# Performance work log

Hardware: AMD Instinct MI355X
Metric: run time of the kernel (lower is better)

The kernel has to match this reference:

```python
import jax, jax.numpy as jnp
import numpy as np

N_NODES = 50000
N_EDGES = 640000
HIDDEN = 128
EDGE_DIM = 32


def _init_linear(key, fan_in, fan_out):
    kw, kb = jax.random.split(key)
    bound = 1.0 / np.sqrt(fan_in)
    W = jax.random.uniform(kw, (fan_in, fan_out), jnp.float32, -bound, bound)
    b = jax.random.uniform(kb, (fan_out,), jnp.float32, -bound, bound)
    return W, b


def setup_inputs() -> dict:
    key = jax.random.key(0)
    ks = jax.random.split(key, 10)
    node_features = jax.random.normal(ks[0], (N_NODES, HIDDEN), jnp.float32)
    edge_index = jax.random.randint(ks[1], (2, N_EDGES), 0, N_NODES, jnp.int64)
    edge_features = jax.random.normal(ks[2], (N_EDGES, EDGE_DIM), jnp.float32)
    coordination = jax.random.uniform(ks[3], (N_NODES,), jnp.float32)
    msg_in = 2 * HIDDEN + EDGE_DIM + 2
    upd_in = 2 * HIDDEN + 1
    mW1, mb1 = _init_linear(ks[4], msg_in, HIDDEN)
    mW2, mb2 = _init_linear(ks[5], HIDDEN, HIDDEN)
    uW1, ub1 = _init_linear(ks[6], upd_in, HIDDEN)
    uW2, ub2 = _init_linear(ks[7], HIDDEN, HIDDEN)
    ln_gamma = jnp.ones((HIDDEN,), jnp.float32)
    ln_beta = jnp.zeros((HIDDEN,), jnp.float32)
    return {
        "node_features": node_features,
        "edge_index": edge_index,
        "edge_features": edge_features,
        "coordination": coordination,
        "mW1": mW1, "mb1": mb1, "mW2": mW2, "mb2": mb2,
        "uW1": uW1, "ub1": ub1, "uW2": uW2, "ub2": ub2,
        "ln_gamma": ln_gamma, "ln_beta": ln_beta,
    }


def _layernorm(x, gamma, beta, eps=1e-5):
    mu = jnp.mean(x, axis=-1, keepdims=True)
    var = jnp.mean(jnp.square(x - mu), axis=-1, keepdims=True)
    return (x - mu) * jax.lax.rsqrt(var + eps) * gamma + beta


def reference(node_features, edge_index, edge_features, coordination,
              mW1, mb1, mW2, mb2, uW1, ub1, uW2, ub2, ln_gamma, ln_beta):
    n_nodes = node_features.shape[0]
    src, dst = edge_index[0], edge_index[1]
    # edge_input: [E, 2H + edge_dim + 2]
    edge_input = jnp.concatenate([
        node_features[src],
        node_features[dst],
        edge_features,
        coordination[src][:, None],
        coordination[dst][:, None],
    ], axis=-1)
    h = jax.nn.silu(edge_input @ mW1 + mb1)
    messages = h @ mW2 + mb2  # [E, H]
    aggregated = jax.ops.segment_sum(messages, dst, num_segments=n_nodes)  # [N, H]
    update_input = jnp.concatenate([
        node_features, aggregated, coordination[:, None]
    ], axis=-1)  # [N, 2H+1]
    u = jax.nn.silu(update_input @ uW1 + ub1)
    upd = u @ uW2 + ub2
    return _layernorm(node_features + upd, ln_gamma, ln_beta)
```

## Files before the change

### kernel.cpp

```cpp
#include <hip/hip_runtime.h>

#define NN 50000
#define NE 640000
#define HID 128


typedef __attribute__((ext_vector_type(8))) short bf8;
typedef __attribute__((ext_vector_type(4))) float f4;

#define MFMA(a, b, c) __builtin_amdgcn_mfma_f32_16x16x32_bf16(a, b, c, 0, 0, 0)

#define SYNC() do { asm volatile("s_waitcnt lgkmcnt(0)" ::: "memory"); \
                    __builtin_amdgcn_s_barrier(); } while (0)

__device__ __forceinline__ short f2bf(float f) {
    union { float f; unsigned u; } v; v.f = f;
    unsigned r = v.u + 0x7FFFu + ((v.u >> 16) & 1u);
    return (short)(r >> 16);
}
__device__ __forceinline__ float bf2f(short s) {
    union { unsigned u; float f; } v; v.u = ((unsigned)(unsigned short)s) << 16;
    return v.f;
}
__device__ __forceinline__ float silu(float x) {
    return x * __builtin_amdgcn_rcpf(1.f + __expf(-x));
}

__global__ __launch_bounds__(256, 2)
void prep_kernel(const float* __restrict__ nf, const float* __restrict__ coord,
                 const float* __restrict__ mW1, const float* __restrict__ mb1,
                 const float* __restrict__ mW2,
                 const float* __restrict__ uW1, const float* __restrict__ uW2,
                 const int* __restrict__ ei,
                 short* __restrict__ W1e, short* __restrict__ W2p,
                 short* __restrict__ U1p, short* __restrict__ U2p,
                 short* __restrict__ Ppre, int* __restrict__ hist) {
    const int b = blockIdx.x, tid = threadIdx.x;
    if (b < 782) {
        __shared__ short SH[64 * 264];
        __shared__ float scoord[64];
        short* A = SH;
        short* P = SH;
        const int nbase = b * 64;

        {
            const int r = tid >> 2, q = tid & 3;
            const int node = nbase + r;
            short* Ar = A + r * 136 + q * 32;
            if (node < NN) {
                const float* p = nf + (long)node * HID + q * 32;
#pragma unroll
                for (int j = 0; j < 4; ++j) {
                    f4 v0 = *(const f4*)(p + j * 8), v1 = *(const f4*)(p + j * 8 + 4);
                    bf8 w = { f2bf(v0[0]), f2bf(v0[1]), f2bf(v0[2]), f2bf(v0[3]),
                              f2bf(v1[0]), f2bf(v1[1]), f2bf(v1[2]), f2bf(v1[3]) };
                    *(bf8*)(Ar + j * 8) = w;
                }
                if (q == 0) scoord[r] = coord[node];
            } else {
                bf8 z = {};
#pragma unroll
                for (int j = 0; j < 4; ++j) *(bf8*)(Ar + j * 8) = z;
                if (q == 0) scoord[r] = 0.f;
            }
        }
        __syncthreads();

        const int lane = tid & 63, wv = tid >> 6;
        const int g = lane >> 4, i16 = lane & 15, wc = wv * 64;

        f4 acc[4][4] = {};
#pragma unroll
        for (int ks = 0; ks < 4; ++ks) {
            const int kb = ks * 32 + g * 8;
            bf8 bfr[4];
#pragma unroll
            for (int n = 0; n < 4; ++n) {
                const int cc = wc + n * 16 + i16;
                const float* wp = mW1 + ((cc >> 7) ? (128 * 128 + (cc - 128)) : cc);
#pragma unroll
                for (int j = 0; j < 8; ++j)
                    bfr[n][j] = f2bf(wp[(kb + j) * 128]);
            }
#pragma unroll
            for (int m = 0; m < 4; ++m) {
                bf8 a = *(const bf8*)(A + (m * 16 + i16) * 136 + kb);
#pragma unroll
                for (int n = 0; n < 4; ++n) acc[m][n] = MFMA(a, bfr[n], acc[m][n]);
            }
        }
        __syncthreads();

#pragma unroll
        for (int n = 0; n < 4; ++n) {
            const int cc = wc + n * 16 + i16;
            const float wa = mW1[(288 + (cc >> 7)) * 128 + (cc & 127)];
            const float ba = (cc >> 7) ? mb1[cc - 128] : 0.f;
#pragma unroll
            for (int m = 0; m < 4; ++m)
#pragma unroll
                for (int i = 0; i < 4; ++i) {
                    const int row = m * 16 + g * 4 + i;
                    P[row * 264 + cc] = f2bf(acc[m][n][i] + scoord[row] * wa + ba);
                }
        }
        __syncthreads();

        {
            const int r = tid >> 2, q = tid & 3;
            const int node = nbase + r;
            if (node < NN) {
#pragma unroll
                for (int j = 0; j < 8; ++j)
                    *(bf8*)(Ppre + (long)node * 256 + q * 64 + j * 8) =
                        *(const bf8*)(P + r * 264 + q * 64 + j * 8);
            }
        }
    } else if (b < 846) {
        const int stride = 64 * 256;
        const int idx = (b - 782) * 256 + tid;
        for (int t = idx; t < 128 * 32; t += stride) {
            int c = t / 32, k = t % 32;
            W1e[t] = f2bf(mW1[(256 + k) * 128 + c]);
        }
        for (int t = idx; t < 128 * 128; t += stride)
            W2p[t] = f2bf(mW2[(t % 128) * 128 + (t / 128)]);
        for (int t = idx; t < 128 * 288; t += stride) {
            int n = t / 288, k = t % 288;
            U1p[t] = (k < 257) ? f2bf(uW1[k * 128 + n]) : (short)0;
        }
        for (int t = idx; t < 128 * 128; t += stride)
            U2p[t] = f2bf(uW2[(t % 128) * 128 + (t / 128)]);
    } else {
        const int stride = 154 * 256;
        for (int e = (b - 846) * 256 + tid; e < NE; e += stride)
            atomicAdd(&hist[ei[NE + e]], 1);
    }
}

__global__ void scan1_kernel(const int* __restrict__ hist, int* __restrict__ pos,
                             int* __restrict__ csum) {
    __shared__ int s[256];
    const int b = blockIdx.x, t = threadIdx.x;
    const int idx = b * 200 + t;
    int v = (t < 200) ? hist[idx] : 0;
    s[t] = v;
    __syncthreads();
    for (int d = 1; d < 256; d <<= 1) {
        int x = (t >= d) ? s[t - d] : 0;
        __syncthreads();
        s[t] += x;
        __syncthreads();
    }
    if (t < 200) pos[idx] = s[t] - v;
    if (t == 255) csum[b] = s[255];
}

__global__ void scan_add_kernel(int* __restrict__ pos, const int* __restrict__ csum) {
    __shared__ int sw[4];
    const int b = blockIdx.x, t = threadIdx.x;
    int v = (t < b) ? csum[t] : 0;
    v += __shfl_xor(v, 1);  v += __shfl_xor(v, 2);  v += __shfl_xor(v, 4);
    v += __shfl_xor(v, 8);  v += __shfl_xor(v, 16); v += __shfl_xor(v, 32);
    if ((t & 63) == 0) sw[t >> 6] = v;
    __syncthreads();
    const int total = sw[0] + sw[1] + sw[2] + sw[3];
    if (t < 200) pos[b * 200 + t] += total;
}

__global__ void scatter_kernel(const int* __restrict__ ei, const float* __restrict__ ef,
                               int* __restrict__ pos, int* __restrict__ srcs,
                               int* __restrict__ dsts, short* __restrict__ efs) {
    const int tid = threadIdx.x;
    const int lane = tid & 63;
    const int r = tid >> 2, q = tid & 3;
#pragma unroll
    for (int k = 0; k < 4; ++k) {
        const int e = (blockIdx.x * 4 + k) * 64 + r;
        int p = 0;
        if (q == 0) {
            const int d = ei[NE + e];
            p = atomicAdd(&pos[d], 1);
            srcs[p] = ei[e];
            dsts[p] = d;
        }
        p = __shfl(p, lane & 60);
        const float* pe = ef + (long)e * 32 + q * 8;
        f4 v0 = *(const f4*)pe, v1 = *(const f4*)(pe + 4);
        bf8 w = { f2bf(v0[0]), f2bf(v0[1]), f2bf(v0[2]), f2bf(v0[3]),
                  f2bf(v1[0]), f2bf(v1[1]), f2bf(v1[2]), f2bf(v1[3]) };
        *(bf8*)(efs + (long)p * 32 + q * 8) = w;
    }
}

__global__ __launch_bounds__(256, 7)
void edge_kernel(const int* __restrict__ srcs, const int* __restrict__ dsts,
                 const short* __restrict__ efs, const short* __restrict__ Ppre,
                 const short* __restrict__ W1e, const short* __restrict__ W2p,
                 const float* __restrict__ mb2, float* __restrict__ agg) {
    constexpr int LDEF = 36, LDH = 136, LDM = 132;
    __shared__ short Aef[64 * LDEF];
    __shared__ short HM[64 * LDH];
    __shared__ int sdst[64], ssrc[64];
    short* H = HM;
    float* Mh = (float*)HM;

    const int tid = threadIdx.x;
    const int bid = blockIdx.x;
    const int ebase = ((bid & 7) * 1250 + (bid >> 3)) * 64;

    const int lane = tid & 63, wv = tid >> 6;
    const int g = lane >> 4, i16 = lane & 15, wc = wv * 32;
    const int r = tid >> 2, q = tid & 3;

    const int e = ebase + r;
    if (q == 0) { sdst[r] = dsts[e]; ssrc[r] = srcs[e]; }
    bf8 ev = *(const bf8*)(efs + (long)e * 32 + q * 8);
    bf8 b0 = *(const bf8*)(W1e + (wc + i16) * 32 + g * 8);
    bf8 b1 = *(const bf8*)(W1e + (wc + 16 + i16) * 32 + g * 8);
    const float c0 = mb2[wc + i16], c1 = mb2[wc + 16 + i16];
    *(bf8*)(Aef + r * LDEF + q * 8) = ev;
    SYNC();

    {
        f4 acc[4][2] = {};
#pragma unroll
        for (int m = 0; m < 4; ++m) {
            bf8 a = *(const bf8*)(Aef + (m * 16 + i16) * LDEF + g * 8);
            acc[m][0] = MFMA(a, b0, acc[m][0]);
            acc[m][1] = MFMA(a, b1, acc[m][1]);
        }
#pragma unroll
        for (int m = 0; m < 4; ++m)
#pragma unroll
            for (int n = 0; n < 2; ++n)
#pragma unroll
                for (int i = 0; i < 4; ++i)
                    H[(m * 16 + g * 4 + i) * LDH + wc + n * 16 + i16] = f2bf(acc[m][n][i]);
    }
    SYNC();

    {
        const int s_ = ssrc[r], d_ = sdst[r];
        const short* p1 = Ppre + (long)s_ * 256 + q * 32;
        const short* p2 = Ppre + (long)d_ * 256 + 128 + q * 32;
        bf8 a1[4], a2[4];
#pragma unroll
        for (int j = 0; j < 4; ++j) a1[j] = *(const bf8*)(p1 + j * 8);
#pragma unroll
        for (int j = 0; j < 4; ++j) a2[j] = *(const bf8*)(p2 + j * 8);
        short* Hr = H + r * LDH + q * 32;
#pragma unroll
        for (int j = 0; j < 4; ++j) {
            bf8 hv = *(const bf8*)(Hr + j * 8);
            bf8 o;
#pragma unroll
            for (int t = 0; t < 8; ++t) {
                float x = bf2f(hv[t]) + bf2f(a1[j][t]) + bf2f(a2[j][t]);
                o[t] = f2bf(silu(x));
            }
            *(bf8*)(Hr + j * 8) = o;
        }
    }
    SYNC();

    f4 acc2[4][2] = {};
#pragma unroll
    for (int ks = 0; ks < 4; ++ks) {
        const int kb = ks * 32 + g * 8;
        bf8 w0 = *(const bf8*)(W2p + (wc + i16) * 128 + kb);
        bf8 w1 = *(const bf8*)(W2p + (wc + 16 + i16) * 128 + kb);
#pragma unroll
        for (int m = 0; m < 4; ++m) {
            bf8 a = *(const bf8*)(H + (m * 16 + i16) * LDH + kb);
            acc2[m][0] = MFMA(a, w0, acc2[m][0]);
            acc2[m][1] = MFMA(a, w1, acc2[m][1]);
        }
    }
    SYNC();

#pragma unroll
    for (int m = 0; m < 2; ++m)
#pragma unroll
        for (int n = 0; n < 2; ++n)
#pragma unroll
            for (int i = 0; i < 4; ++i)
                Mh[(m * 16 + g * 4 + i) * LDM + wc + n * 16 + i16] =
                    acc2[m][n][i] + (n ? c1 : c0);
    SYNC();
    {
        const int col = tid & 127, half = tid >> 7;
        const int base = half * 16;
        float run = 0.f;
#pragma unroll
        for (int rr = 0; rr < 16; ++rr) {
            const int row = base + rr;
            run += Mh[row * LDM + col];
            const bool last = (rr == 15) || (sdst[row + 1] != sdst[row]);
            if (last) {
                atomicAdd(agg + (long)sdst[row] * HID + col, run);
                run = 0.f;
            }
        }
    }
    SYNC();

#pragma unroll
    for (int m = 2; m < 4; ++m)
#pragma unroll
        for (int n = 0; n < 2; ++n)
#pragma unroll
            for (int i = 0; i < 4; ++i)
                Mh[((m - 2) * 16 + g * 4 + i) * LDM + wc + n * 16 + i16] =
                    acc2[m][n][i] + (n ? c1 : c0);
    SYNC();
    {
        const int col = tid & 127, half = tid >> 7;
        const int base = half * 16;
        float run = 0.f;
#pragma unroll
        for (int rr = 0; rr < 16; ++rr) {
            const int row = 32 + base + rr;
            run += Mh[(row - 32) * LDM + col];
            const bool last = (rr == 15) || (row == 63) || (sdst[row + 1] != sdst[row]);
            if (last) {
                atomicAdd(agg + (long)sdst[row] * HID + col, run);
                run = 0.f;
            }
        }
    }
}

__global__ __launch_bounds__(256, 4)
void node_kernel(const float* __restrict__ nf, const float* __restrict__ agg,
                 const float* __restrict__ coord,
                 const short* __restrict__ U1p, const float* __restrict__ ub1,
                 const short* __restrict__ U2p, const float* __restrict__ ub2,
                 const float* __restrict__ gamma, const float* __restrict__ beta,
                 float* __restrict__ out) {
    constexpr int K1 = 288, LDA = 296, LDH = 136, LDX = 132;
    __shared__ short SH[64 * LDA];
    short* A = SH;
    short* H = SH;
    float* X = (float*)SH;

    const int tid = threadIdx.x;
    const int nbase = blockIdx.x * 64;

    {
        const int r = tid >> 2, q = tid & 3;
        const int node = nbase + r;
        short* Ar = A + r * LDA;
        bf8 z = {};
        if (node < NN) {
            const float* pn = nf + (long)node * HID + q * 32;
            const float* pa = agg + (long)node * HID + q * 32;
#pragma unroll
            for (int j = 0; j < 4; ++j) {
                f4 v0 = *(const f4*)(pn + j * 8), v1 = *(const f4*)(pn + j * 8 + 4);
                bf8 w = { f2bf(v0[0]), f2bf(v0[1]), f2bf(v0[2]), f2bf(v0[3]),
                          f2bf(v1[0]), f2bf(v1[1]), f2bf(v1[2]), f2bf(v1[3]) };
                *(bf8*)(Ar + q * 32 + j * 8) = w;
            }
#pragma unroll
            for (int j = 0; j < 4; ++j) {
                f4 v0 = *(const f4*)(pa + j * 8), v1 = *(const f4*)(pa + j * 8 + 4);
                bf8 w = { f2bf(v0[0]), f2bf(v0[1]), f2bf(v0[2]), f2bf(v0[3]),
                          f2bf(v1[0]), f2bf(v1[1]), f2bf(v1[2]), f2bf(v1[3]) };
                *(bf8*)(Ar + 128 + q * 32 + j * 8) = w;
            }
            *(bf8*)(Ar + 256 + q * 8) = z;
            if (q == 0) Ar[256] = f2bf(coord[node]);
        } else {
#pragma unroll
            for (int j = 0; j < 4; ++j) {
                *(bf8*)(Ar + q * 32 + j * 8) = z;
                *(bf8*)(Ar + 128 + q * 32 + j * 8) = z;
            }
            *(bf8*)(Ar + 256 + q * 8) = z;
        }
    }
    SYNC();

    const int lane = tid & 63, wv = tid >> 6;
    const int g = lane >> 4, i16 = lane & 15, wc = wv * 32;

    f4 acc[4][2] = {};
#pragma unroll
    for (int ks = 0; ks < K1 / 32; ++ks) {
        const int kb = ks * 32 + g * 8;
        bf8 b0 = *(const bf8*)(U1p + (wc + i16) * K1 + kb);
        bf8 b1 = *(const bf8*)(U1p + (wc + 16 + i16) * K1 + kb);
#pragma unroll
        for (int m = 0; m < 4; ++m) {
            bf8 a = *(const bf8*)(A + (m * 16 + i16) * LDA + kb);
            acc[m][0] = MFMA(a, b0, acc[m][0]);
            acc[m][1] = MFMA(a, b1, acc[m][1]);
        }
    }
    SYNC();

    {
        const float c0 = ub1[wc + i16], c1 = ub1[wc + 16 + i16];
#pragma unroll
        for (int m = 0; m < 4; ++m)
#pragma unroll
            for (int n = 0; n < 2; ++n)
#pragma unroll
                for (int i = 0; i < 4; ++i) {
                    float x = acc[m][n][i] + (n ? c1 : c0);
                    H[(m * 16 + g * 4 + i) * LDH + wc + n * 16 + i16] = f2bf(silu(x));
                }
    }
    SYNC();

    f4 acc2[4][2] = {};
#pragma unroll
    for (int ks = 0; ks < 4; ++ks) {
        const int kb = ks * 32 + g * 8;
        bf8 b0 = *(const bf8*)(U2p + (wc + i16) * 128 + kb);
        bf8 b1 = *(const bf8*)(U2p + (wc + 16 + i16) * 128 + kb);
#pragma unroll
        for (int m = 0; m < 4; ++m) {
            bf8 a = *(const bf8*)(H + (m * 16 + i16) * LDH + kb);
            acc2[m][0] = MFMA(a, b0, acc2[m][0]);
            acc2[m][1] = MFMA(a, b1, acc2[m][1]);
        }
    }
    SYNC();

    {
        const float c0 = ub2[wc + i16], c1 = ub2[wc + 16 + i16];
#pragma unroll
        for (int m = 0; m < 4; ++m)
#pragma unroll
            for (int n = 0; n < 2; ++n)
#pragma unroll
                for (int i = 0; i < 4; ++i) {
                    const int row = m * 16 + g * 4 + i;
                    const int node = nbase + row;
                    const int col = wc + n * 16 + i16;
                    float v = acc2[m][n][i] + (n ? c1 : c0);
                    float base = (node < NN) ? nf[(long)node * HID + col] : 0.f;
                    X[row * LDX + col] = base + v;
                }
    }
    SYNC();

    {
        const int r = tid >> 2, q = tid & 3;
        const int node = nbase + r;
        float s = 0.f;
#pragma unroll
        for (int j = 0; j < 32; ++j) s += X[r * LDX + q * 32 + j];
        s += __shfl_xor(s, 1);
        s += __shfl_xor(s, 2);
        const float mu = s * (1.f / 128.f);
        float vv = 0.f;
#pragma unroll
        for (int j = 0; j < 32; ++j) {
            float d = X[r * LDX + q * 32 + j] - mu;
            vv += d * d;
        }
        vv += __shfl_xor(vv, 1);
        vv += __shfl_xor(vv, 2);
        const float rstd = rsqrtf(vv * (1.f / 128.f) + 1e-5f);
        if (node < NN) {
#pragma unroll
            for (int j = 0; j < 32; ++j) {
                const int c = q * 32 + j;
                out[(long)node * HID + c] = (X[r * LDX + c] - mu) * rstd * gamma[c] + beta[c];
            }
        }
    }
}

extern "C" void kernel_launch(void* const* d_in, const int* in_sizes, int n_in,
                              void* d_out, int out_size, void* d_ws, size_t ws_size,
                              hipStream_t stream) {
    const float* nf    = (const float*)d_in[0];
    const int*   ei    = (const int*)d_in[1];
    const float* ef    = (const float*)d_in[2];
    const float* coord = (const float*)d_in[3];
    const float* mW1 = (const float*)d_in[4];
    const float* mb1 = (const float*)d_in[5];
    const float* mW2 = (const float*)d_in[6];
    const float* mb2 = (const float*)d_in[7];
    const float* uW1 = (const float*)d_in[8];
    const float* ub1 = (const float*)d_in[9];
    const float* uW2 = (const float*)d_in[10];
    const float* ub2 = (const float*)d_in[11];
    const float* gamma = (const float*)d_in[12];
    const float* beta  = (const float*)d_in[13];
    float* out = (float*)d_out;

    char* ws = (char*)d_ws;
    float* agg  = (float*)ws;
    int*   hist = (int*)(ws + 25600000);
    short* W1e  = (short*)(ws + 25800000);
    short* W2p  = (short*)(ws + 25808192);
    short* U1p  = (short*)(ws + 25840960);
    short* U2p  = (short*)(ws + 25914688);
    int*   pos  = (int*)(ws + 25947456);
    int*   csum = (int*)(ws + 26147456);
    int*   srcs = (int*)(ws + 26148480);
    int*   dsts = (int*)(ws + 28708480);
    short* efs  = (short*)(ws + 31268480);
    short* Ppre = (short*)d_out;

    hipMemsetAsync(ws, 0, 25800000, stream);
    prep_kernel<<<1000, 256, 0, stream>>>(nf, coord, mW1, mb1, mW2, uW1, uW2, ei,
                                          W1e, W2p, U1p, U2p, Ppre, hist);
    scan1_kernel<<<250, 256, 0, stream>>>(hist, pos, csum);
    scan_add_kernel<<<250, 256, 0, stream>>>(pos, csum);
    scatter_kernel<<<2500, 256, 0, stream>>>(ei, ef, pos, srcs, dsts, efs);
    edge_kernel<<<NE / 64, 256, 0, stream>>>(srcs, dsts, efs, Ppre, W1e, W2p, mb2, agg);
    node_kernel<<<782, 256, 0, stream>>>(nf, agg, coord,
                                         U1p, ub1, U2p, ub2, gamma, beta, out);
}
```

Baseline: 219.4 us.

## Split node precompute into its own kernel using prepacked bf16 weights

The node-level message precompute is moved out of the combined prep kernel into a separate kernel. The 782 precompute blocks previously converted mW1 columns from strided fp32 global reads to bf16 on every block; they now load a bf16 weight matrix packed once by the prep kernel. That packed buffer reuses the edge-feature scratch region, so the new kernel must run before the scatter kernel overwrites it. The change also drops a redundant boundary check in the edge aggregation loop and adds one kernel launch.

```diff
diff --git a/kernel.cpp b/kernel.cpp
--- a/kernel.cpp
+++ b/kernel.cpp
@@ -26,99 +26,22 @@
     return x * __builtin_amdgcn_rcpf(1.f + __expf(-x));
 }
 
-__global__ __launch_bounds__(256, 2)
-void prep_kernel(const float* __restrict__ nf, const float* __restrict__ coord,
-                 const float* __restrict__ mW1, const float* __restrict__ mb1,
-                 const float* __restrict__ mW2,
-                 const float* __restrict__ uW1, const float* __restrict__ uW2,
-                 const int* __restrict__ ei,
-                 short* __restrict__ W1e, short* __restrict__ W2p,
-                 short* __restrict__ U1p, short* __restrict__ U2p,
-                 short* __restrict__ Ppre, int* __restrict__ hist) {
+__global__ __launch_bounds__(256)
+void pack_hist_kernel(const float* __restrict__ mW1, const float* __restrict__ mW2,
+                      const float* __restrict__ uW1, const float* __restrict__ uW2,
+                      const int* __restrict__ ei,
+                      short* __restrict__ Wpre, short* __restrict__ W1e,
+                      short* __restrict__ W2p, short* __restrict__ U1p,
+                      short* __restrict__ U2p, int* __restrict__ hist) {
     const int b = blockIdx.x, tid = threadIdx.x;
-    if (b < 782) {
-        __shared__ short SH[64 * 264];
-        __shared__ float scoord[64];
-        short* A = SH;
-        short* P = SH;
-        const int nbase = b * 64;
-
-        {
-            const int r = tid >> 2, q = tid & 3;
-            const int node = nbase + r;
-            short* Ar = A + r * 136 + q * 32;
-            if (node < NN) {
-                const float* p = nf + (long)node * HID + q * 32;
-#pragma unroll
-                for (int j = 0; j < 4; ++j) {
-                    f4 v0 = *(const f4*)(p + j * 8), v1 = *(const f4*)(p + j * 8 + 4);
-                    bf8 w = { f2bf(v0[0]), f2bf(v0[1]), f2bf(v0[2]), f2bf(v0[3]),
-                              f2bf(v1[0]), f2bf(v1[1]), f2bf(v1[2]), f2bf(v1[3]) };
-                    *(bf8*)(Ar + j * 8) = w;
-                }
-                if (q == 0) scoord[r] = coord[node];
-            } else {
-                bf8 z = {};
-#pragma unroll
-                for (int j = 0; j < 4; ++j) *(bf8*)(Ar + j * 8) = z;
-                if (q == 0) scoord[r] = 0.f;
-            }
-        }
-        __syncthreads();
-
-        const int lane = tid & 63, wv = tid >> 6;
-        const int g = lane >> 4, i16 = lane & 15, wc = wv * 64;
-
-        f4 acc[4][4] = {};
-#pragma unroll
-        for (int ks = 0; ks < 4; ++ks) {
-            const int kb = ks * 32 + g * 8;
-            bf8 bfr[4];
-#pragma unroll
-            for (int n = 0; n < 4; ++n) {
-                const int cc = wc + n * 16 + i16;
-                const float* wp = mW1 + ((cc >> 7) ? (128 * 128 + (cc - 128)) : cc);
-#pragma unroll
-                for (int j = 0; j < 8; ++j)
-                    bfr[n][j] = f2bf(wp[(kb + j) * 128]);
-            }
-#pragma unroll
-            for (int m = 0; m < 4; ++m) {
-                bf8 a = *(const bf8*)(A + (m * 16 + i16) * 136 + kb);
-#pragma unroll
-                for (int n = 0; n < 4; ++n) acc[m][n] = MFMA(a, bfr[n], acc[m][n]);
-            }
-        }
-        __syncthreads();
-
-#pragma unroll
-        for (int n = 0; n < 4; ++n) {
-            const int cc = wc + n * 16 + i16;
-            const float wa = mW1[(288 + (cc >> 7)) * 128 + (cc & 127)];
-            const float ba = (cc >> 7) ? mb1[cc - 128] : 0.f;
-#pragma unroll
-            for (int m = 0; m < 4; ++m)
-#pragma unroll
-                for (int i = 0; i < 4; ++i) {
-                    const int row = m * 16 + g * 4 + i;
-                    P[row * 264 + cc] = f2bf(acc[m][n][i] + scoord[row] * wa + ba);
-                }
-        }
-        __syncthreads();
-
-        {
-            const int r = tid >> 2, q = tid & 3;
-            const int node = nbase + r;
-            if (node < NN) {
-#pragma unroll
-                for (int j = 0; j < 8; ++j)
-                    *(bf8*)(Ppre + (long)node * 256 + q * 64 + j * 8) =
-                        *(const bf8*)(P + r * 264 + q * 64 + j * 8);
-            }
-        }
-    } else if (b < 846) {
+    if (b < 64) {
         const int stride = 64 * 256;
-        const int idx = (b - 782) * 256 + tid;
+        const int idx = b * 256 + tid;
+        for (int t = idx; t < 256 * 128; t += stride) {
+            int cc = t / 128, k = t % 128;
+            float v = (cc < 128) ? mW1[k * 128 + cc] : mW1[(128 + k) * 128 + (cc - 128)];
+            Wpre[t] = f2bf(v);
+        }
         for (int t = idx; t < 128 * 32; t += stride) {
             int c = t / 32, k = t % 32;
             W1e[t] = f2bf(mW1[(256 + k) * 128 + c]);
@@ -132,9 +55,90 @@
         for (int t = idx; t < 128 * 128; t += stride)
             U2p[t] = f2bf(uW2[(t % 128) * 128 + (t / 128)]);
     } else {
-        const int stride = 154 * 256;
-        for (int e = (b - 846) * 256 + tid; e < NE; e += stride)
+        const int stride = 192 * 256;
+        for (int e = (b - 64) * 256 + tid; e < NE; e += stride)
             atomicAdd(&hist[ei[NE + e]], 1);
+    }
+}
+
+__global__ __launch_bounds__(256, 3)
+void node_pre_kernel(const float* __restrict__ nf, const float* __restrict__ coord,
+                     const short* __restrict__ Wpre, const float* __restrict__ mW1,
+                     const float* __restrict__ mb1, short* __restrict__ Ppre) {
+    __shared__ short SH[64 * 264];
+    __shared__ float scoord[64];
+    short* A = SH;
+    short* P = SH;
+    const int tid = threadIdx.x;
+    const int nbase = blockIdx.x * 64;
+
+    {
+        const int r = tid >> 2, q = tid & 3;
+        const int node = nbase + r;
+        short* Ar = A + r * 136 + q * 32;
+        if (node < NN) {
+            const float* p = nf + (long)node * HID + q * 32;
+#pragma unroll
+            for (int j = 0; j < 4; ++j) {
+                f4 v0 = *(const f4*)(p + j * 8), v1 = *(const f4*)(p + j * 8 + 4);
+                bf8 w = { f2bf(v0[0]), f2bf(v0[1]), f2bf(v0[2]), f2bf(v0[3]),
+                          f2bf(v1[0]), f2bf(v1[1]), f2bf(v1[2]), f2bf(v1[3]) };
+                *(bf8*)(Ar + j * 8) = w;
+            }
+            if (q == 0) scoord[r] = coord[node];
+        } else {
+            bf8 z = {};
+#pragma unroll
+            for (int j = 0; j < 4; ++j) *(bf8*)(Ar + j * 8) = z;
+            if (q == 0) scoord[r] = 0.f;
+        }
+    }
+    __syncthreads();
+
+    const int lane = tid & 63, wv = tid >> 6;
+    const int g = lane >> 4, i16 = lane & 15, wc = wv * 64;
+
+    f4 acc[4][4] = {};
+#pragma unroll
+    for (int ks = 0; ks < 4; ++ks) {
+        const int kb = ks * 32 + g * 8;
+        bf8 b[4];
+#pragma unroll
+        for (int n = 0; n < 4; ++n)
+            b[n] = *(const bf8*)(Wpre + (wc + n * 16 + i16) * 128 + kb);
+#pragma unroll
+        for (int m = 0; m < 4; ++m) {
+            bf8 a = *(const bf8*)(A + (m * 16 + i16) * 136 + kb);
+#pragma unroll
+            for (int n = 0; n < 4; ++n) acc[m][n] = MFMA(a, b[n], acc[m][n]);
+        }
+    }
+    __syncthreads();
+
+#pragma unroll
+    for (int n = 0; n < 4; ++n) {
+        const int cc = wc + n * 16 + i16;
+        const float wa = mW1[(288 + (cc >> 7)) * 128 + (cc & 127)];
+        const float ba = (cc >> 7) ? mb1[cc - 128] : 0.f;
+#pragma unroll
+        for (int m = 0; m < 4; ++m)
+#pragma unroll
+            for (int i = 0; i < 4; ++i) {
+                const int row = m * 16 + g * 4 + i;
+                P[row * 264 + cc] = f2bf(acc[m][n][i] + scoord[row] * wa + ba);
+            }
+    }
+    __syncthreads();
+
+    {
+        const int r = tid >> 2, q = tid & 3;
+        const int node = nbase + r;
+        if (node < NN) {
+#pragma unroll
+            for (int j = 0; j < 8; ++j)
+                *(bf8*)(Ppre + (long)node * 256 + q * 64 + j * 8) =
+                    *(const bf8*)(P + r * 264 + q * 64 + j * 8);
+        }
     }
 }
 
@@ -322,7 +326,7 @@
         for (int rr = 0; rr < 16; ++rr) {
             const int row = 32 + base + rr;
             run += Mh[(row - 32) * LDM + col];
-            const bool last = (rr == 15) || (row == 63) || (sdst[row + 1] != sdst[row]);
+            const bool last = (rr == 15) || (sdst[row + 1] != sdst[row]);
             if (last) {
                 atomicAdd(agg + (long)sdst[row] * HID + col, run);
                 run = 0.f;
@@ -506,13 +510,15 @@
     int*   srcs = (int*)(ws + 26148480);
     int*   dsts = (int*)(ws + 28708480);
     short* efs  = (short*)(ws + 31268480);
+    short* Wpre = efs;
     short* Ppre = (short*)d_out;
 
     hipMemsetAsync(ws, 0, 25800000, stream);
-    prep_kernel<<<1000, 256, 0, stream>>>(nf, coord, mW1, mb1, mW2, uW1, uW2, ei,
-                                          W1e, W2p, U1p, U2p, Ppre, hist);
+    pack_hist_kernel<<<256, 256, 0, stream>>>(mW1, mW2, uW1, uW2, ei,
+                                              Wpre, W1e, W2p, U1p, U2p, hist);
     scan1_kernel<<<250, 256, 0, stream>>>(hist, pos, csum);
     scan_add_kernel<<<250, 256, 0, stream>>>(pos, csum);
+    node_pre_kernel<<<782, 256, 0, stream>>>(nf, coord, Wpre, mW1, mb1, Ppre);
     scatter_kernel<<<2500, 256, 0, stream>>>(ei, ef, pos, srcs, dsts, efs);
     edge_kernel<<<NE / 64, 256, 0, stream>>>(srcs, dsts, efs, Ppre, W1e, W2p, mb2, agg);
     node_kernel<<<782, 256, 0, stream>>>(nf, agg, coord,
```

New measurement: 231.7 us. +5.6%, slower.
